# Kernel tuning notes

Measured on AMD Instinct MI355X. Metric: run time of the kernel, lower is better.

## Reference

```python
import math
import jax, jax.numpy as jnp
import numpy as np

N_HEAD = 32
HEAD_DIM = 64
ROTARY_DIM = 32
ROTARY_BASE = 10000.0


def _rope(u, cos, sin):
    # u: [B, S, H, head_dim]; cos/sin: [S, ROTARY_DIM//2]
    u_rot = u[..., :ROTARY_DIM].astype(jnp.float32)
    u1, u2 = jnp.split(u_rot, 2, axis=-1)          # [B,S,H,rot/2] each
    c = cos[None, :, None, :]
    s = sin[None, :, None, :]
    r = jnp.concatenate([u1 * c - u2 * s, u1 * s + u2 * c], axis=-1).astype(u.dtype)
    return jnp.concatenate([r, u[..., ROTARY_DIM:]], axis=-1)


def setup_inputs() -> dict:
    key = jax.random.key(0)
    ks = jax.random.split(key, 5)
    B, S, D = 2, 2048, 2048
    std = 1.0 / math.sqrt(D)
    x = jax.random.normal(ks[0], (B, S, D), dtype=jnp.float32)
    Wqkv = jax.random.normal(ks[1], (D, 3 * D), dtype=jnp.float32) * std
    b_qkv = jax.random.normal(ks[2], (3 * D,), dtype=jnp.float32) * 0.01
    Wout = jax.random.normal(ks[3], (D, D), dtype=jnp.float32) * std
    b_out = jax.random.normal(ks[4], (D,), dtype=jnp.float32) * 0.01
    return {"x": x, "Wqkv": Wqkv, "b_qkv": b_qkv, "Wout": Wout, "b_out": b_out}


def reference(x, Wqkv, b_qkv, Wout, b_out):
    B, S, D = x.shape
    H, hd = N_HEAD, HEAD_DIM
    # QKV projection -> [B, S, 3, H, hd]
    qkv = (x @ Wqkv + b_qkv).reshape(B, S, 3, H, hd)
    # Rotary cos/sin cache (fp32 position indices, as in the module)
    inv_freq = 1.0 / (ROTARY_BASE ** (jnp.arange(0, ROTARY_DIM, 2, dtype=jnp.float32) / ROTARY_DIM))
    t = jnp.arange(S, dtype=jnp.float32)
    freqs = jnp.outer(t, inv_freq)                 # [S, ROTARY_DIM//2]
    cos, sin = jnp.cos(freqs), jnp.sin(freqs)
    q = _rope(qkv[:, :, 0], cos, sin)
    k = _rope(qkv[:, :, 1], cos, sin)
    v = qkv[:, :, 2]
    scale = 1.0 / math.sqrt(hd)
    scores = jnp.einsum('bthd,bshd->bhts', q, k * scale)   # [B,H,S,S]
    rows = jnp.arange(S)[:, None]
    cols = jnp.arange(S)[None, :]
    causal_mask = cols > rows                      # seqlen_k == seqlen_q here
    scores = jnp.where(causal_mask[None, None], jnp.asarray(-10000.0, scores.dtype), scores)
    attn = jax.nn.softmax(scores, axis=-1)         # dropout p=0.0
    out = jnp.einsum('bhts,bshd->bthd', attn, v).reshape(B, S, D)
    return out @ Wout + b_out
```

## Files before the change

kernel.cpp:

```cpp
#include <hip/hip_runtime.h>
#include <stdint.h>
#include <math.h>

#define DEV static __device__ __forceinline__

typedef __attribute__((ext_vector_type(8))) short bf16x8;
typedef __attribute__((ext_vector_type(4))) float f32x4;
typedef __attribute__((ext_vector_type(8))) unsigned short u16x8;
typedef __attribute__((ext_vector_type(4))) unsigned short u16x4;
typedef __attribute__((ext_vector_type(2))) unsigned int u32x2;

enum { B_ = 2, S_ = 2048, D_ = 2048, H_ = 32, HD_ = 64, N3_ = 6144, M_ = 4096 };

DEV unsigned short f2bf(float f) {
  unsigned u = __float_as_uint(f);
  u += 0x7FFFu + ((u >> 16) & 1u);
  return (unsigned short)(u >> 16);
}
DEV float bf2f(unsigned short s) { return __uint_as_float(((unsigned)s) << 16); }

DEV void load16(const void* g, void* l) {
  __builtin_amdgcn_global_load_lds((const __attribute__((address_space(1))) void*)g,
                                   (__attribute__((address_space(3))) void*)l,
                                   16, 0, 0);
}

DEV f32x4 mfma16(bf16x8 a, bf16x8 b, f32x4 c) {
  return __builtin_amdgcn_mfma_f32_16x16x32_bf16(a, b, c, 0, 0, 0);
}

__global__ __launch_bounds__(256) void cvt_bf16(const float* __restrict__ in,
                                                unsigned short* __restrict__ out, int n) {
  int i = blockIdx.x * 256 + threadIdx.x;
  if (i * 8 >= n) return;
  const float4* in4 = (const float4*)in;
  float4 a = in4[i * 2 + 0];
  float4 b = in4[i * 2 + 1];
  u16x8 o;
  o[0] = f2bf(a.x); o[1] = f2bf(a.y); o[2] = f2bf(a.z); o[3] = f2bf(a.w);
  o[4] = f2bf(b.x); o[5] = f2bf(b.y); o[6] = f2bf(b.z); o[7] = f2bf(b.w);
  *(u16x8*)(out + (size_t)i * 8) = o;
}

__global__ __launch_bounds__(256) void transpose_bf16(const float* __restrict__ W,
                                                      unsigned short* __restrict__ Wt,
                                                      int Kg, int Ng) {
  __shared__ float tile[32][33];
  const int tn = blockIdx.x, tk = blockIdx.y;
  const int t = threadIdx.x;
  const int r = t >> 3, c4 = (t & 7) * 4;
  float4 v = *(const float4*)(W + (size_t)(tk * 32 + r) * Ng + tn * 32 + c4);
  tile[r][c4 + 0] = v.x; tile[r][c4 + 1] = v.y;
  tile[r][c4 + 2] = v.z; tile[r][c4 + 3] = v.w;
  __syncthreads();
  u16x4 o;
  o[0] = f2bf(tile[c4 + 0][r]);
  o[1] = f2bf(tile[c4 + 1][r]);
  o[2] = f2bf(tile[c4 + 2][r]);
  o[3] = f2bf(tile[c4 + 3][r]);
  *(u16x4*)(Wt + (size_t)(tn * 32 + r) * Kg + tk * 32 + c4) = o;
}

__global__ __launch_bounds__(256, 2) void gemm_qkv(const unsigned short* __restrict__ A,
                                                   const unsigned short* __restrict__ BT,
                                                   const float* __restrict__ bias,
                                                   unsigned short* __restrict__ Oqk,
                                                   unsigned short* __restrict__ vt,
                                                   int Mg, int Ng, int Kg) {
  __shared__ __align__(16) char lds[81920];
  const int tid = threadIdx.x;
  const int lane = tid & 63, w = tid >> 6;
  const int g = (lane >> 4) & 3, l16 = lane & 15;
  const int wn = w;

  const int wg = (blockIdx.x & 7) * (gridDim.x >> 3) + (blockIdx.x >> 3);
  const int nTM = Mg >> 7;
  const int tm = wg % nTM, tn = wg / nTM;
  const int rb = tm * 128, cb = tn * 192;
  const int NT = Kg >> 6;

  int c0, c1, c2;
  if (wn == 0)      { c0 = 0;   c1 = 16;  c2 = 32;  }
  else if (wn == 1) { c0 = 64;  c1 = 80;  c2 = 48;  }
  else if (wn == 2) { c0 = 128; c1 = 144; c2 = 96;  }
  else              { c0 = 112; c1 = 160; c2 = 176; }

  const int su0 = (g ^ (l16 & 7)) * 16;
  const int su1 = ((4 + g) ^ (l16 & 7)) * 16;
  const int offA = l16 * 128;
  const int offB0 = 16384 + (c0 + l16) * 128;
  const int offB1 = 16384 + (c1 + l16) * 128;
  const int offB2 = 16384 + (c2 + l16) * 128;

  const int r0 = tid >> 3;
  const int u8e = ((tid & 7) ^ (r0 & 7)) * 8;
  const unsigned short* sAa = A + (size_t)(rb + r0) * Kg + u8e;
  const unsigned short* sBb = BT + (size_t)(cb + r0) * Kg + u8e;
  const size_t rs32 = (size_t)Kg * 32;
  const int dstb = tid * 16;

  auto SA0 = [&](int t) { char* db = (char*)lds + ((t & 1) ? 40960 : 0);
    load16(sAa + (size_t)t * 64, db + dstb);
    load16(sAa + rs32 + (size_t)t * 64, db + 4096 + dstb); };
  auto SA1 = [&](int t) { char* db = (char*)lds + ((t & 1) ? 40960 : 0);
    load16(sAa + 2 * rs32 + (size_t)t * 64, db + 8192 + dstb);
    load16(sAa + 3 * rs32 + (size_t)t * 64, db + 12288 + dstb); };
  auto SB = [&](int t) { char* db = (char*)lds + ((t & 1) ? 40960 : 0) + 16384;
#pragma unroll
    for (int c = 0; c < 6; ++c)
      load16(sBb + c * rs32 + (size_t)t * 64, db + c * 4096 + dstb); };

  SA0(0); SA1(0); SB(0); SA0(1); SB(1);
  asm volatile("s_waitcnt vmcnt(8)" ::: "memory");
  __builtin_amdgcn_s_barrier();

  f32x4 acc[8][3] = {};
  bf16x8 a[4][2], b[3][2];

  for (int t = 0; t < NT; ++t) {
    const char* bs = (const char*)lds + ((t & 1) ? 40960 : 0);
#pragma unroll
    for (int mf = 0; mf < 4; ++mf) {
      a[mf][0] = *(const bf16x8*)(bs + offA + mf * 2048 + su0);
      a[mf][1] = *(const bf16x8*)(bs + offA + mf * 2048 + su1);
    }
    b[0][0] = *(const bf16x8*)(bs + offB0 + su0);
    b[0][1] = *(const bf16x8*)(bs + offB0 + su1);
    b[1][0] = *(const bf16x8*)(bs + offB1 + su0);
    b[1][1] = *(const bf16x8*)(bs + offB1 + su1);
    b[2][0] = *(const bf16x8*)(bs + offB2 + su0);
    b[2][1] = *(const bf16x8*)(bs + offB2 + su1);
    if (t + 1 < NT) SA1(t + 1);
    asm volatile("s_waitcnt lgkmcnt(8)" ::: "memory");
    __builtin_amdgcn_s_barrier();
    asm volatile("s_waitcnt lgkmcnt(0)" ::: "memory");
    __builtin_amdgcn_s_setprio(1);
#pragma unroll
    for (int mf = 0; mf < 4; ++mf)
#pragma unroll
      for (int nf = 0; nf < 3; ++nf)
#pragma unroll
        for (int kh = 0; kh < 2; ++kh)
          acc[mf][nf] = mfma16(a[mf][kh], b[nf][kh], acc[mf][nf]);
    __builtin_amdgcn_s_setprio(0);
    __builtin_amdgcn_s_barrier();
    if (t == NT - 1) asm volatile("s_waitcnt vmcnt(0)" ::: "memory");
    else             asm volatile("s_waitcnt vmcnt(10)" ::: "memory");
#pragma unroll
    for (int mf = 0; mf < 4; ++mf) {
      a[mf][0] = *(const bf16x8*)(bs + offA + (mf + 4) * 2048 + su0);
      a[mf][1] = *(const bf16x8*)(bs + offA + (mf + 4) * 2048 + su1);
    }
    if (t + 2 < NT) { SA0(t + 2); SB(t + 2); }
    __builtin_amdgcn_s_barrier();
    asm volatile("s_waitcnt lgkmcnt(0)" ::: "memory");
    __builtin_amdgcn_s_setprio(1);
#pragma unroll
    for (int mf = 0; mf < 4; ++mf)
#pragma unroll
      for (int nf = 0; nf < 3; ++nf)
#pragma unroll
        for (int kh = 0; kh < 2; ++kh)
          acc[mf + 4][nf] = mfma16(a[mf][kh], b[nf][kh], acc[mf + 4][nf]);
    __builtin_amdgcn_s_setprio(0);
    if (t + 2 < NT)      asm volatile("s_waitcnt vmcnt(10)" ::: "memory");
    else if (t + 1 < NT) asm volatile("s_waitcnt vmcnt(2)" ::: "memory");
    __builtin_amdgcn_s_barrier();
  }

  const int crow0 = rb + g * 4;
  const float bv0 = bias[cb + c0 + l16];
  const float bv1 = bias[cb + c1 + l16];
  const float bv2 = bias[cb + c2 + l16];
  const bool rotp = (wn < 3) && (cb + c0 < 4096);
  const float invf = exp2f(-(float)l16 * 0.83048202372184056f);

#define STOREG(NF, CG, BV) do {                                                \
    const int col0_ = cb + (CG);                                               \
    if (col0_ >= 4096) {                                                       \
      const int hv_ = (col0_ - 4096) >> 6;                                     \
      const int dd_ = (col0_ & 63) + l16;                                      \
      _Pragma("unroll")                                                        \
      for (int mf = 0; mf < 8; ++mf) {                                         \
        int rowb_ = crow0 + mf * 16;                                           \
        int bb_ = rowb_ >> 11, s0_ = rowb_ & (S_ - 1);                         \
        u16x4 ov_;                                                             \
        _Pragma("unroll")                                                      \
        for (int r = 0; r < 4; ++r) ov_[r] = f2bf(acc[mf][NF][r] + (BV));      \
        *(u16x4*)(vt + ((size_t)(bb_ * 32 + hv_) * 64 + dd_) * S_ + s0_) = ov_;\
      }                                                                        \
    } else {                                                                   \
      _Pragma("unroll")                                                        \
      for (int mf = 0; mf < 8; ++mf)                                           \
        _Pragma("unroll")                                                      \
        for (int r = 0; r < 4; ++r) {                                          \
          int row_ = crow0 + mf * 16 + r;                                      \
          Oqk[(size_t)row_ * Ng + col0_ + l16] = f2bf(acc[mf][NF][r] + (BV));  \
        }                                                                      \
    }                                                                          \
  } while (0)

  if (rotp) {
#pragma unroll
    for (int mf = 0; mf < 8; ++mf)
#pragma unroll
      for (int r = 0; r < 4; ++r) {
        int row = crow0 + mf * 16 + r;
        float v0 = acc[mf][0][r] + bv0;
        float v1 = acc[mf][1][r] + bv1;
        float ang = (float)(row & (S_ - 1)) * invf;
        float sn = __sinf(ang), cs = __cosf(ang);
        float t0 = v0 * cs - v1 * sn;
        v1 = v0 * sn + v1 * cs;
        unsigned short* p = Oqk + (size_t)row * Ng;
        p[cb + c0 + l16] = f2bf(t0);
        p[cb + c1 + l16] = f2bf(v1);
      }
  } else {
    STOREG(0, c0, bv0);
    STOREG(1, c1, bv1);
  }
  STOREG(2, c2, bv2);
#undef STOREG
}

DEV int xsw(int row) { return (row ^ (row >> 2)) & 3; }

__global__ __launch_bounds__(256) void gemm_bt_f32(const unsigned short* __restrict__ A,
                                                   const unsigned short* __restrict__ BT,
                                                   const float* __restrict__ bias,
                                                   float* __restrict__ Cout,
                                                   int Mg, int Ng, int Kg) {
  __shared__ __align__(16) unsigned short lA[128 * 32];
  __shared__ __align__(16) unsigned short lB[128 * 32];
  const int tid = threadIdx.x;
  const int lane = tid & 63, wv = tid >> 6;
  const int g = lane >> 4, l16 = lane & 15;
  const int wr = wv >> 1, wc = wv & 1;
  const int rb = blockIdx.x * 128, cb = blockIdx.y * 128;

  f32x4 acc[4][4] = {};

  for (int k0 = 0; k0 < Kg; k0 += 32) {
    __syncthreads();
#pragma unroll
    for (int c = 0; c < 2; ++c) {
      int p = c * 256 + tid;
      int row = p >> 2;
      int k8l = (p & 3) ^ xsw(row);
      load16(A + (size_t)(rb + row) * Kg + k0 + 8 * k8l, (char*)lA + p * 16);
      load16(BT + (size_t)(cb + row) * Kg + k0 + 8 * k8l, (char*)lB + p * 16);
    }
    __syncthreads();
    bf16x8 af[4], bfr[4];
#pragma unroll
    for (int m = 0; m < 4; ++m) {
      int row = wr * 64 + m * 16 + l16;
      af[m] = *(const bf16x8*)((const char*)lA + (size_t)(row * 4 + (g ^ xsw(row))) * 16);
    }
#pragma unroll
    for (int n = 0; n < 4; ++n) {
      int row = wc * 64 + n * 16 + l16;
      bfr[n] = *(const bf16x8*)((const char*)lB + (size_t)(row * 4 + (g ^ xsw(row))) * 16);
    }
#pragma unroll
    for (int m = 0; m < 4; ++m)
#pragma unroll
      for (int n = 0; n < 4; ++n)
        acc[m][n] = mfma16(af[m], bfr[n], acc[m][n]);
  }

  const int ccol0 = cb + wc * 64 + l16;
  float bv[4];
#pragma unroll
  for (int n = 0; n < 4; ++n) bv[n] = bias[ccol0 + n * 16];
#pragma unroll
  for (int m = 0; m < 4; ++m)
#pragma unroll
    for (int r = 0; r < 4; ++r) {
      int row = rb + wr * 64 + m * 16 + g * 4 + r;
      float* p = Cout + (size_t)row * Ng + ccol0;
      p[0] = acc[m][0][r] + bv[0];
      p[16] = acc[m][1][r] + bv[1];
      p[32] = acc[m][2][r] + bv[2];
      p[48] = acc[m][3][r] + bv[3];
    }
}

DEV void stage_kv(const unsigned short* __restrict__ qkv,
                  const unsigned short* __restrict__ vt,
                  unsigned char* lds, int bS, int bh64, int hoff, int kvb, int buf, int tid) {
#pragma unroll
  for (int c = 0; c < 2; ++c) {
    int p = c * 256 + tid;
    int row = p >> 3, k8 = (p & 7) ^ (row & 7);
    load16(qkv + (size_t)(bS + kvb + row) * N3_ + 2048 + hoff + 8 * k8,
           lds + buf * 8192 + p * 16);
    load16(vt + (size_t)(bh64 + row) * S_ + kvb + 8 * k8,
           lds + 16384 + buf * 8192 + p * 16);
  }
}

__global__ __launch_bounds__(256, 3) void attn_kernel(const unsigned short* __restrict__ qkv,
                                                      const unsigned short* __restrict__ vt,
                                                      unsigned short* __restrict__ ao) {
  __shared__ __align__(16) unsigned char lds[49152];
  const int tid = threadIdx.x;
  const int lane = tid & 63, wv = tid >> 6;
  const int g = lane >> 4, l16 = lane & 15;
  const int bid = blockIdx.x;
  const int qi = 15 - (bid >> 6);
  const int t6 = bid & 63;
  const int bh = ((t6 & 7) << 3) | (t6 >> 3);
  const int b = bh >> 5, h = bh & 31;
  const int qbase = qi * 128;
  const int srow0 = qbase + wv * 32;
  const int bS = b * S_, bh64 = bh * 64, hoff = h * 64;

  bf16x8 qf[2][2];
#pragma unroll
  for (int m = 0; m < 2; ++m)
#pragma unroll
    for (int kt = 0; kt < 2; ++kt)
      qf[m][kt] = *(const bf16x8*)(qkv + (size_t)(bS + srow0 + m * 16 + l16) * N3_ +
                                   hoff + kt * 32 + g * 8);

  float mrun[2] = {-INFINITY, -INFINITY}, lrun[2] = {0.f, 0.f};
  f32x4 o[2][4] = {};
  unsigned char* pw = lds + 32768 + wv * 4096;

  const int nkv = (qbase + 128) >> 6;
  stage_kv(qkv, vt, lds, bS, bh64, hoff, 0, 0, tid);
  __syncthreads();

  for (int kb = 0; kb < nkv; ++kb) {
    const int cur = kb & 1;
    if (kb + 1 < nkv) stage_kv(qkv, vt, lds, bS, bh64, hoff, (kb + 1) << 6, cur ^ 1, tid);
    const int kvb = kb << 6;
    if (kvb <= srow0 + 31) {
      const unsigned char* kbuf = lds + cur * 8192;
      const unsigned char* vbuf = lds + 16384 + cur * 8192;

      f32x4 sc[2][4];
#pragma unroll
      for (int n = 0; n < 4; ++n) {
        int row = n * 16 + l16;
        bf16x8 kf0 = *(const bf16x8*)(kbuf + (row * 8 + ((g + 0) ^ (row & 7))) * 16);
        bf16x8 kf1 = *(const bf16x8*)(kbuf + (row * 8 + ((g + 4) ^ (row & 7))) * 16);
#pragma unroll
        for (int m = 0; m < 2; ++m) {
          f32x4 z = {};
          z = mfma16(kf0, qf[m][0], z);
          z = mfma16(kf1, qf[m][1], z);
          sc[m][n] = z;
        }
      }

      const bool boundary = (kvb + 63 > srow0);
#pragma unroll
      for (int m = 0; m < 2; ++m) {
        const int qrow = srow0 + m * 16 + l16;
        if (boundary) {
#pragma unroll
          for (int n = 0; n < 4; ++n)
#pragma unroll
            for (int r = 0; r < 4; ++r) {
              int k = kvb + n * 16 + g * 4 + r;
              if (k > qrow) sc[m][n][r] = -INFINITY;
            }
        }
        float mx = fmaxf(fmaxf(sc[m][0][0], sc[m][0][1]), fmaxf(sc[m][0][2], sc[m][0][3]));
#pragma unroll
        for (int n = 1; n < 4; ++n)
          mx = fmaxf(mx, fmaxf(fmaxf(sc[m][n][0], sc[m][n][1]), fmaxf(sc[m][n][2], sc[m][n][3])));
        mx = fmaxf(mx, __shfl_xor(mx, 16));
        mx = fmaxf(mx, __shfl_xor(mx, 32));
        float pm = mx * 0.125f;
        if (!__all(pm <= mrun[m] + 8.0f)) {
          float mn = fmaxf(mrun[m], pm);
          float al = exp2f((mrun[m] - mn) * 1.44269504f);
          mrun[m] = mn; lrun[m] *= al;
#pragma unroll
          for (int d = 0; d < 4; ++d) o[m][d] *= al;
        }
        const float mt = mrun[m] * 1.44269504f;
        float p[4][4]; float rs = 0.f;
#pragma unroll
        for (int n = 0; n < 4; ++n)
#pragma unroll
          for (int r = 0; r < 4; ++r) {
            p[n][r] = exp2f(fmaf(sc[m][n][r], 0.18033688011112042f, -mt));
            rs += p[n][r];
          }
        rs += __shfl_xor(rs, 16);
        rs += __shfl_xor(rs, 32);
        lrun[m] += rs;
#pragma unroll
        for (int n = 0; n < 4; ++n) {
          unsigned lo, hi;
          asm("v_cvt_pk_bf16_f32 %0, %1, %2" : "=v"(lo) : "v"(p[n][0]), "v"(p[n][1]));
          asm("v_cvt_pk_bf16_f32 %0, %1, %2" : "=v"(hi) : "v"(p[n][2]), "v"(p[n][3]));
          int su = (n * 4 + g) ^ ((l16 & 7) << 1);
          u32x2 wq; wq[0] = lo; wq[1] = hi;
          *(u32x2*)(pw + ((m * 16 + l16) * 16 + su) * 8) = wq;
        }
      }

      bf16x8 pf[2][2];
#pragma unroll
      for (int m = 0; m < 2; ++m)
#pragma unroll
        for (int kt = 0; kt < 2; ++kt) {
          int su = (kt * 8 + g * 2) ^ ((l16 & 7) << 1);
          pf[m][kt] = *(const bf16x8*)(pw + ((m * 16 + l16) * 16 + su) * 8);
        }
#pragma unroll
      for (int dblk = 0; dblk < 4; ++dblk) {
        int row = dblk * 16 + l16;
        bf16x8 vf0 = *(const bf16x8*)(vbuf + (row * 8 + ((g + 0) ^ (row & 7))) * 16);
        bf16x8 vf1 = *(const bf16x8*)(vbuf + (row * 8 + ((g + 4) ^ (row & 7))) * 16);
#pragma unroll
        for (int m = 0; m < 2; ++m) {
          o[m][dblk] = mfma16(vf0, pf[m][0], o[m][dblk]);
          o[m][dblk] = mfma16(vf1, pf[m][1], o[m][dblk]);
        }
      }
    }
    __syncthreads();
  }

#pragma unroll
  for (int m = 0; m < 2; ++m) {
    float inv = 1.0f / lrun[m];
    int q = srow0 + m * 16 + l16;
#pragma unroll
    for (int dblk = 0; dblk < 4; ++dblk) {
      u16x4 ov;
#pragma unroll
      for (int r = 0; r < 4; ++r) ov[r] = f2bf(o[m][dblk][r] * inv);
      *(u16x4*)(ao + (size_t)(bS + q) * D_ + hoff + dblk * 16 + g * 4) = ov;
    }
  }
}

extern "C" void kernel_launch(void* const* d_in, const int* in_sizes, int n_in,
                              void* d_out, int out_size, void* d_ws, size_t ws_size,
                              hipStream_t stream) {
  const float* x = (const float*)d_in[0];
  const float* Wqkv = (const float*)d_in[1];
  const float* bqkv = (const float*)d_in[2];
  const float* Wout = (const float*)d_in[3];
  const float* bout = (const float*)d_in[4];
  float* out = (float*)d_out;

  char* ws = (char*)d_ws;
  unsigned short* Xb = (unsigned short*)(ws + 0);
  unsigned short* Wqkvt = (unsigned short*)(ws + 16777216);
  unsigned short* Woutt = (unsigned short*)(ws + 41943040);
  unsigned short* QKVb = (unsigned short*)(ws + 50331648);
  unsigned short* Vt = (unsigned short*)(ws + 100663296);
  unsigned short* AO = Xb;

  cvt_bf16<<<4096, 256, 0, stream>>>(x, Xb, M_ * D_);
  transpose_bf16<<<dim3(192, 64), 256, 0, stream>>>(Wqkv, Wqkvt, 2048, 6144);
  transpose_bf16<<<dim3(64, 64), 256, 0, stream>>>(Wout, Woutt, 2048, 2048);
  gemm_qkv<<<1024, 256, 0, stream>>>(Xb, Wqkvt, bqkv, QKVb, Vt, M_, N3_, D_);
  attn_kernel<<<1024, 256, 0, stream>>>(QKVb, Vt, AO);
  gemm_bt_f32<<<dim3(32, 16), 256, 0, stream>>>(AO, Woutt, bout, out, M_, D_, D_);
}
```

Before: 254.9 us.

## Replace output-projection GEMM with double-buffered pipelined kernel modeled on QKV GEMM

The simple output GEMM, which synced twice per K-step of 32, is replaced by a kernel with K-step 64, two LDS buffers, split A/B staging issued ahead, manual waitcnt/barrier scheduling, setprio around MFMA blocks and a grouped tile order for L2 locality. The aim is to hide global-load latency behind MFMA work in the final projection. The QKV GEMM also moves a barrier to after the vmcnt wait, which fixes ordering so staged data is complete before other waves read it. This uses 64KB of LDS per block, which limits occupancy to about two blocks per CU.

Result: faster. 236.3 us (-7.3%).

```diff
diff --git a/kernel.cpp b/kernel.cpp
--- a/kernel.cpp
+++ b/kernel.cpp
@@ -143,9 +143,9 @@
         for (int kh = 0; kh < 2; ++kh)
           acc[mf][nf] = mfma16(a[mf][kh], b[nf][kh], acc[mf][nf]);
     __builtin_amdgcn_s_setprio(0);
-    __builtin_amdgcn_s_barrier();
     if (t == NT - 1) asm volatile("s_waitcnt vmcnt(0)" ::: "memory");
     else             asm volatile("s_waitcnt vmcnt(10)" ::: "memory");
+    __builtin_amdgcn_s_barrier();
 #pragma unroll
     for (int mf = 0; mf < 4; ++mf) {
       a[mf][0] = *(const bf16x8*)(bs + offA + (mf + 4) * 2048 + su0);
@@ -224,66 +224,115 @@
 #undef STOREG
 }
 
-DEV int xsw(int row) { return (row ^ (row >> 2)) & 3; }
-
-__global__ __launch_bounds__(256) void gemm_bt_f32(const unsigned short* __restrict__ A,
+__global__ __launch_bounds__(256, 2) void gemm_out(const unsigned short* __restrict__ A,
                                                    const unsigned short* __restrict__ BT,
                                                    const float* __restrict__ bias,
                                                    float* __restrict__ Cout,
                                                    int Mg, int Ng, int Kg) {
-  __shared__ __align__(16) unsigned short lA[128 * 32];
-  __shared__ __align__(16) unsigned short lB[128 * 32];
+  __shared__ __align__(16) char lds[65536];
   const int tid = threadIdx.x;
-  const int lane = tid & 63, wv = tid >> 6;
-  const int g = lane >> 4, l16 = lane & 15;
-  const int wr = wv >> 1, wc = wv & 1;
-  const int rb = blockIdx.x * 128, cb = blockIdx.y * 128;
-
-  f32x4 acc[4][4] = {};
-
-  for (int k0 = 0; k0 < Kg; k0 += 32) {
-    __syncthreads();
-#pragma unroll
-    for (int c = 0; c < 2; ++c) {
-      int p = c * 256 + tid;
-      int row = p >> 2;
-      int k8l = (p & 3) ^ xsw(row);
-      load16(A + (size_t)(rb + row) * Kg + k0 + 8 * k8l, (char*)lA + p * 16);
-      load16(BT + (size_t)(cb + row) * Kg + k0 + 8 * k8l, (char*)lB + p * 16);
-    }
-    __syncthreads();
-    bf16x8 af[4], bfr[4];
-#pragma unroll
-    for (int m = 0; m < 4; ++m) {
-      int row = wr * 64 + m * 16 + l16;
-      af[m] = *(const bf16x8*)((const char*)lA + (size_t)(row * 4 + (g ^ xsw(row))) * 16);
-    }
-#pragma unroll
-    for (int n = 0; n < 4; ++n) {
-      int row = wc * 64 + n * 16 + l16;
-      bfr[n] = *(const bf16x8*)((const char*)lB + (size_t)(row * 4 + (g ^ xsw(row))) * 16);
-    }
-#pragma unroll
-    for (int m = 0; m < 4; ++m)
-#pragma unroll
-      for (int n = 0; n < 4; ++n)
-        acc[m][n] = mfma16(af[m], bfr[n], acc[m][n]);
+  const int lane = tid & 63, w = tid >> 6;
+  const int g = (lane >> 4) & 3, l16 = lane & 15;
+  const int wn = w;
+
+  const int wg = (blockIdx.x & 7) * (gridDim.x >> 3) + (blockIdx.x >> 3);
+  const int nTM = Mg >> 7;
+  const int tm = wg % nTM, tn = wg / nTM;
+  const int rb = tm * 128, cb = tn * 128;
+  const int NT = Kg >> 6;
+
+  const int su0 = (g ^ (l16 & 7)) * 16;
+  const int su1 = ((4 + g) ^ (l16 & 7)) * 16;
+  const int offA = l16 * 128;
+  const int offB0 = 16384 + (wn * 32 + l16) * 128;
+  const int offB1 = offB0 + 2048;
+
+  const int r0 = tid >> 3;
+  const int u8e = ((tid & 7) ^ (r0 & 7)) * 8;
+  const unsigned short* sAa = A + (size_t)(rb + r0) * Kg + u8e;
+  const unsigned short* sBb = BT + (size_t)(cb + r0) * Kg + u8e;
+  const size_t rs32 = (size_t)Kg * 32;
+  const int dstb = tid * 16;
+
+  auto SA0 = [&](int t) { char* db = (char*)lds + ((t & 1) ? 32768 : 0);
+    load16(sAa + (size_t)t * 64, db + dstb);
+    load16(sAa + rs32 + (size_t)t * 64, db + 4096 + dstb); };
+  auto SA1 = [&](int t) { char* db = (char*)lds + ((t & 1) ? 32768 : 0);
+    load16(sAa + 2 * rs32 + (size_t)t * 64, db + 8192 + dstb);
+    load16(sAa + 3 * rs32 + (size_t)t * 64, db + 12288 + dstb); };
+  auto SB = [&](int t) { char* db = (char*)lds + ((t & 1) ? 32768 : 0) + 16384;
+#pragma unroll
+    for (int c = 0; c < 4; ++c)
+      load16(sBb + c * rs32 + (size_t)t * 64, db + c * 4096 + dstb); };
+
+  SA0(0); SA1(0); SB(0); SA0(1); SB(1);
+  asm volatile("s_waitcnt vmcnt(6)" ::: "memory");
+  __builtin_amdgcn_s_barrier();
+
+  f32x4 acc[8][2] = {};
+  bf16x8 a[4][2], b[2][2];
+
+  for (int t = 0; t < NT; ++t) {
+    const char* bs = (const char*)lds + ((t & 1) ? 32768 : 0);
+#pragma unroll
+    for (int mf = 0; mf < 4; ++mf) {
+      a[mf][0] = *(const bf16x8*)(bs + offA + mf * 2048 + su0);
+      a[mf][1] = *(const bf16x8*)(bs + offA + mf * 2048 + su1);
+    }
+    b[0][0] = *(const bf16x8*)(bs + offB0 + su0);
+    b[0][1] = *(const bf16x8*)(bs + offB0 + su1);
+    b[1][0] = *(const bf16x8*)(bs + offB1 + su0);
+    b[1][1] = *(const bf16x8*)(bs + offB1 + su1);
+    if (t + 1 < NT) SA1(t + 1);
+    asm volatile("s_waitcnt lgkmcnt(8)" ::: "memory");
+    __builtin_amdgcn_s_barrier();
+    asm volatile("s_waitcnt lgkmcnt(0)" ::: "memory");
+    __builtin_amdgcn_s_setprio(1);
+#pragma unroll
+    for (int mf = 0; mf < 4; ++mf)
+#pragma unroll
+      for (int nf = 0; nf < 2; ++nf)
+#pragma unroll
+        for (int kh = 0; kh < 2; ++kh)
+          acc[mf][nf] = mfma16(a[mf][kh], b[nf][kh], acc[mf][nf]);
+    __builtin_amdgcn_s_setprio(0);
+    if (t == NT - 1) asm volatile("s_waitcnt vmcnt(0)" ::: "memory");
+    else             asm volatile("s_waitcnt vmcnt(8)" ::: "memory");
+    __builtin_amdgcn_s_barrier();
+#pragma unroll
+    for (int mf = 0; mf < 4; ++mf) {
+      a[mf][0] = *(const bf16x8*)(bs + offA + (mf + 4) * 2048 + su0);
+      a[mf][1] = *(const bf16x8*)(bs + offA + (mf + 4) * 2048 + su1);
+    }
+    if (t + 2 < NT) { SA0(t + 2); SB(t + 2); }
+    __builtin_amdgcn_s_barrier();
+    asm volatile("s_waitcnt lgkmcnt(0)" ::: "memory");
+    __builtin_amdgcn_s_setprio(1);
+#pragma unroll
+    for (int mf = 0; mf < 4; ++mf)
+#pragma unroll
+      for (int nf = 0; nf < 2; ++nf)
+#pragma unroll
+        for (int kh = 0; kh < 2; ++kh)
+          acc[mf + 4][nf] = mfma16(a[mf][kh], b[nf][kh], acc[mf + 4][nf]);
+    __builtin_amdgcn_s_setprio(0);
+    if (t + 2 < NT)      asm volatile("s_waitcnt vmcnt(8)" ::: "memory");
+    else if (t + 1 < NT) asm volatile("s_waitcnt vmcnt(2)" ::: "memory");
+    __builtin_amdgcn_s_barrier();
   }
 
-  const int ccol0 = cb + wc * 64 + l16;
-  float bv[4];
-#pragma unroll
-  for (int n = 0; n < 4; ++n) bv[n] = bias[ccol0 + n * 16];
-#pragma unroll
-  for (int m = 0; m < 4; ++m)
+  const int crow0 = rb + g * 4;
+  const int ccol0 = cb + wn * 32 + l16;
+  const float bv0 = bias[ccol0];
+  const float bv1 = bias[ccol0 + 16];
+#pragma unroll
+  for (int mf = 0; mf < 8; ++mf)
 #pragma unroll
     for (int r = 0; r < 4; ++r) {
-      int row = rb + wr * 64 + m * 16 + g * 4 + r;
+      int row = crow0 + mf * 16 + r;
       float* p = Cout + (size_t)row * Ng + ccol0;
-      p[0] = acc[m][0][r] + bv[0];
-      p[16] = acc[m][1][r] + bv[1];
-      p[32] = acc[m][2][r] + bv[2];
-      p[48] = acc[m][3][r] + bv[3];
+      p[0] = acc[mf][0][r] + bv0;
+      p[16] = acc[mf][1][r] + bv1;
     }
 }
 
@@ -466,5 +515,5 @@
   transpose_bf16<<<dim3(64, 64), 256, 0, stream>>>(Wout, Woutt, 2048, 2048);
   gemm_qkv<<<1024, 256, 0, stream>>>(Xb, Wqkvt, bqkv, QKVb, Vt, M_, N3_, D_);
   attn_kernel<<<1024, 256, 0, stream>>>(QKVb, Vt, AO);
-  gemm_bt_f32<<<dim3(32, 16), 256, 0, stream>>>(AO, Woutt, bout, out, M_, D_, D_);
-}
+  gemm_out<<<512, 256, 0, stream>>>(AO, Woutt, bout, out, M_, D_, D_);
+}
```
